# Optimization experiments

Measured on AMD Instinct MI355X. Metric: run time of the kernel, lower is better.

The kernel has to match this reference:

```python
import jax, jax.numpy as jnp
import numpy as np

B = 384          # batch; must equal F for the final broadcast to be valid
F = 384          # out_features
H = 64           # hidden_dim
TAU = 1.0        # d_k passed to attention()
EPS = 1e-12      # F.normalize eps


def _l2_normalize(x):
    # torch F.normalize(p=2, dim=-1): x / max(||x||, eps)
    n = jnp.sqrt(jnp.sum(x * x, axis=-1, keepdims=True))
    return x / jnp.maximum(n, EPS)


def setup_inputs() -> dict:
    key = jax.random.key(0)
    kx, kwq, kbq, kwk, kbk = jax.random.split(key, 5)
    bound = 1.0 / np.sqrt(F)  # torch Linear default init range
    x = jax.random.normal(kx, (B, F), dtype=jnp.float32)
    Wq = jax.random.uniform(kwq, (F * H, F), jnp.float32, -bound, bound)
    bq = jax.random.uniform(kbq, (F * H,), jnp.float32, -bound, bound)
    Wk = jax.random.uniform(kwk, (F * H, F), jnp.float32, -bound, bound)
    bk = jax.random.uniform(kbk, (F * H,), jnp.float32, -bound, bound)
    return {"x": x, "Wq": Wq, "bq": bq, "Wk": Wk, "bk": bk}


def reference(x, Wq, bq, Wk, bk):
    # q = qs(x), k = ks(x): [B, F*H] -> reshape [B, F, H]
    q = (x @ Wq.T + bq).reshape(B, F, H)
    k = (x @ Wk.T + bk).reshape(B, F, H)
    # L2-normalized QK attention with temperature sqrt(tau)
    q = _l2_normalize(q)
    k = _l2_normalize(k)
    scores = jnp.einsum('bfh,bgh->bfg', q, k) / jnp.sqrt(jnp.float32(TAU))
    scores = jax.nn.softmax(scores, axis=-1)  # [B, F, F]
    # faithful to `input * scores`: x[B,F] left-pads to [1,B,F]; valid since B==F
    return x * scores
```

## Files before the change

### kernel.cpp

```cpp
#include <hip/hip_runtime.h>
#include <hip/hip_bf16.h>


typedef __attribute__((ext_vector_type(8))) short bf16x8;
typedef __attribute__((ext_vector_type(4))) float f32x4;

__device__ __forceinline__ ushort f2bf(float f) {
  union { __hip_bfloat16 h; ushort u; } c;
  c.h = __float2bfloat16(f);
  return c.u;
}

__device__ __forceinline__ void load_lds16(const void* g, void* l) {
  __builtin_amdgcn_global_load_lds(
      (const __attribute__((address_space(1))) void*)g,
      (__attribute__((address_space(3))) void*)l, 16, 0, 0);
}

__global__ __launch_bounds__(256) void xconv(const float* __restrict__ xin,
                                             ushort* __restrict__ xbf) {
  int t = blockIdx.x * 256 + threadIdx.x;
  int o = t * 8;
  int kt = o / 12288;
  int rem = o - kt * 12288;
  int m = rem >> 5;
  int sp = (rem >> 3) & 3;
  int slot = sp ^ ((m >> 1) & 3);
  const float* src = xin + m * 384 + kt * 32 + slot * 8;
  float4 a = *reinterpret_cast<const float4*>(src);
  float4 b = *reinterpret_cast<const float4*>(src + 4);
  ushort4 u0 = make_ushort4(f2bf(a.x), f2bf(a.y), f2bf(a.z), f2bf(a.w));
  ushort4 u1 = make_ushort4(f2bf(b.x), f2bf(b.y), f2bf(b.z), f2bf(b.w));
  *reinterpret_cast<ushort4*>(xbf + o)     = u0;
  *reinterpret_cast<ushort4*>(xbf + o + 4) = u1;
}

__global__ __launch_bounds__(256) void qk_gemm(
    const ushort* __restrict__ xbf,
    const float* __restrict__ Wq, const float* __restrict__ bq,
    const float* __restrict__ Wk, const float* __restrict__ bk,
    ushort* __restrict__ qhat, ushort* __restrict__ khat)
{
  const int bx = blockIdx.x;
  const int n0 = bx * 64;
  const float* W    = blockIdx.y ? Wk : Wq;
  const float* bias = blockIdx.y ? bk : bq;
  ushort* outp      = blockIdx.y ? khat : qhat;

  __shared__ __align__(16) ushort Alds[384 * 32];
  __shared__ __align__(16) ushort Blds[64 * 40];

  const int tid  = threadIdx.x;
  const int wave = tid >> 6;
  const int lane = tid & 63;
  const int l15  = lane & 15;
  const int lhi  = lane >> 4;

  f32x4 acc[6][4];
  #pragma unroll
  for (int m = 0; m < 6; ++m)
    #pragma unroll
    for (int n = 0; n < 4; ++n) acc[m][n] = (f32x4)(0.f);

  const int aslot = lhi ^ ((l15 >> 1) & 3);

  for (int kt = 0; kt < 12; ++kt) {
    const ushort* asrc = xbf + kt * 12288 + lane * 8;
    #pragma unroll
    for (int i = 0; i < 6; ++i) {
      int chunk = wave * 6 + i;
      load_lds16(asrc + chunk * 512, (char*)Alds + chunk * 1024);
    }
    #pragma unroll
    for (int i = 0; i < 2; ++i) {
      int idx = tid + 256 * i;
      int row = idx >> 3, c4 = idx & 7;
      float4 v = *reinterpret_cast<const float4*>(
          W + (size_t)(n0 + row) * 384 + kt * 32 + c4 * 4);
      ushort4 u = make_ushort4(f2bf(v.x), f2bf(v.y), f2bf(v.z), f2bf(v.w));
      *reinterpret_cast<ushort4*>(&Blds[row * 40 + c4 * 4]) = u;
    }
    __syncthreads();

    bf16x8 bfr[4];
    #pragma unroll
    for (int nf = 0; nf < 4; ++nf)
      bfr[nf] = *reinterpret_cast<const bf16x8*>(&Blds[(nf * 16 + l15) * 40 + lhi * 8]);
    #pragma unroll
    for (int mf = 0; mf < 6; ++mf) {
      int rr = wave * 96 + mf * 16 + l15;
      bf16x8 afr = *reinterpret_cast<const bf16x8*>(&Alds[rr * 32 + aslot * 8]);
      #pragma unroll
      for (int nf = 0; nf < 4; ++nf)
        acc[mf][nf] = __builtin_amdgcn_mfma_f32_16x16x32_bf16(afr, bfr[nf], acc[mf][nf], 0, 0, 0);
    }
    __syncthreads();
  }

  float bv[4];
  #pragma unroll
  for (int nf = 0; nf < 4; ++nf) bv[nf] = bias[n0 + nf * 16 + l15];

  float scl[6][4];
  #pragma unroll
  for (int mf = 0; mf < 6; ++mf) {
    float ss[4];
    #pragma unroll
    for (int j = 0; j < 4; ++j) {
      float s = 0.f;
      #pragma unroll
      for (int nf = 0; nf < 4; ++nf) {
        float v = acc[mf][nf][j] + bv[nf];
        acc[mf][nf][j] = v;
        s += v * v;
      }
      ss[j] = s;
    }
    #pragma unroll
    for (int m = 1; m < 16; m <<= 1) {
      #pragma unroll
      for (int j = 0; j < 4; ++j) ss[j] += __shfl_xor(ss[j], m, 64);
    }
    #pragma unroll
    for (int j = 0; j < 4; ++j)
      scl[mf][j] = 1.f / fmaxf(sqrtf(ss[j]), 1e-12f);
  }

  const int sw = bx & 7;
  ushort* E = Alds + wave * 3072;
  #pragma unroll
  for (int hh = 0; hh < 2; ++hh) {
    __syncthreads();
    #pragma unroll
    for (int lmf = 0; lmf < 3; ++lmf) {
      const int mf = hh * 3 + lmf;
      #pragma unroll
      for (int nf = 0; nf < 4; ++nf)
        #pragma unroll
        for (int j = 0; j < 4; ++j)
          E[(lmf * 16 + lhi * 4 + j) * 64 + nf * 16 + l15] =
              f2bf(acc[mf][nf][j] * scl[mf][j]);
    }
    __syncthreads();
    #pragma unroll
    for (int i = 0; i < 6; ++i) {
      int lr = i * 8 + (lane >> 3);
      int q  = lane & 7;
      bf16x8 v = *reinterpret_cast<const bf16x8*>(&E[lr * 64 + ((q ^ sw) << 3)]);
      int grow = wave * 96 + hh * 48 + lr;
      *reinterpret_cast<bf16x8*>(outp + (size_t)grow * 24576 + n0 + q * 8) = v;
    }
  }
}

#define PSTR 392
__global__ __launch_bounds__(256, 3) void attn_out(
    const float* __restrict__ xin,
    const ushort* __restrict__ qhat,
    const ushort* __restrict__ khat,
    float* __restrict__ out)
{
  const int id  = blockIdx.x;
  const int xcd = id & 7;
  const int j_  = id >> 3;
  const int b   = xcd * 48 + j_ / 6;
  const int f0  = (j_ % 6) * 64;

  __shared__ __align__(16) char smem[32 * PSTR * 4];
  ushort* Klds = reinterpret_cast<ushort*>(smem);
  float*  Slds = reinterpret_cast<float*>(smem);

  const int tid  = threadIdx.x;
  const int wave = tid >> 6;
  const int lane = tid & 63;
  const int l15  = lane & 15;
  const int lhi  = lane >> 4;

  const int fr = f0 + wave * 16 + l15;
  bf16x8 q8[2];
  #pragma unroll
  for (int ks = 0; ks < 2; ++ks)
    q8[ks] = *reinterpret_cast<const bf16x8*>(
        qhat + (size_t)b * 24576 + (size_t)fr * 64 + (((ks * 4 + lhi) ^ (l15 & 7)) << 3));
  __builtin_amdgcn_sched_barrier(0);

  const ushort* ksrc = khat + (size_t)b * 24576 + lane * 8;
  #pragma unroll
  for (int i = 0; i < 6; ++i) {
    int chunk = wave + 4 * i;
    load_lds16(ksrc + chunk * 512, (char*)Klds + chunk * 1024);
  }
  __builtin_amdgcn_sched_barrier(0);
  #pragma unroll
  for (int i = 6; i < 12; ++i) {
    int chunk = wave + 4 * i;
    load_lds16(ksrc + chunk * 512, (char*)Klds + chunk * 1024);
  }

  f32x4 acc[24];
  #pragma unroll
  for (int n = 0; n < 24; ++n) acc[n] = (f32x4)(0.f);

  asm volatile("s_waitcnt vmcnt(6)" ::: "memory");
  __builtin_amdgcn_s_barrier();
  __builtin_amdgcn_sched_barrier(0);
  #pragma unroll
  for (int ks = 0; ks < 2; ++ks) {
    #pragma unroll
    for (int nf = 0; nf < 12; ++nf) {
      bf16x8 kf = *reinterpret_cast<const bf16x8*>(
          &Klds[(nf * 16 + l15) * 64 + (((ks * 4 + lhi) ^ (l15 & 7)) << 3)]);
      acc[nf] = __builtin_amdgcn_mfma_f32_16x16x32_bf16(kf, q8[ks], acc[nf], 0, 0, 0);
    }
  }
  asm volatile("s_waitcnt vmcnt(0)" ::: "memory");
  __builtin_amdgcn_s_barrier();
  __builtin_amdgcn_sched_barrier(0);
  #pragma unroll
  for (int ks = 0; ks < 2; ++ks) {
    #pragma unroll
    for (int nf = 12; nf < 24; ++nf) {
      bf16x8 kf = *reinterpret_cast<const bf16x8*>(
          &Klds[(nf * 16 + l15) * 64 + (((ks * 4 + lhi) ^ (l15 & 7)) << 3)]);
      acc[nf] = __builtin_amdgcn_mfma_f32_16x16x32_bf16(kf, q8[ks], acc[nf], 0, 0, 0);
    }
  }

  float m0 = acc[0][0], m1 = acc[0][1], m2 = acc[0][2], m3 = acc[0][3];
  #pragma unroll
  for (int nf = 1; nf < 24; ++nf) {
    m0 = fmaxf(m0, acc[nf][0]); m1 = fmaxf(m1, acc[nf][1]);
    m2 = fmaxf(m2, acc[nf][2]); m3 = fmaxf(m3, acc[nf][3]);
  }
  float m = fmaxf(fmaxf(m0, m1), fmaxf(m2, m3));
  m = fmaxf(m, __shfl_xor(m, 16, 64));
  m = fmaxf(m, __shfl_xor(m, 32, 64));

  float s0 = 0.f, s1 = 0.f, s2 = 0.f, s3 = 0.f;
  #pragma unroll
  for (int nf = 0; nf < 24; ++nf) {
    float p0 = __expf(acc[nf][0] - m);
    float p1 = __expf(acc[nf][1] - m);
    float p2 = __expf(acc[nf][2] - m);
    float p3 = __expf(acc[nf][3] - m);
    acc[nf][0] = p0; acc[nf][1] = p1; acc[nf][2] = p2; acc[nf][3] = p3;
    s0 += p0; s1 += p1; s2 += p2; s3 += p3;
  }
  float s = (s0 + s1) + (s2 + s3);
  s += __shfl_xor(s, 16, 64);
  s += __shfl_xor(s, 32, 64);
  const float inv = 1.f / s;

  __syncthreads();

  #pragma unroll
  for (int half = 0; half < 2; ++half) {
    if ((wave >> 1) == half) {
      const int prow = (wave & 1) * 16 + l15;
      #pragma unroll
      for (int nf = 0; nf < 24; ++nf) {
        f32x4 v;
        v[0] = acc[nf][0] * inv; v[1] = acc[nf][1] * inv;
        v[2] = acc[nf][2] * inv; v[3] = acc[nf][3] * inv;
        *reinterpret_cast<f32x4*>(&Slds[prow * PSTR + nf * 16 + lhi * 4]) = v;
      }
    }
    __syncthreads();

    const int rbase = f0 + half * 32;
    const float* xsrc = xin + (size_t)rbase * 384;
    float* odst = out + (size_t)b * 147456 + (size_t)rbase * 384;
    #pragma unroll
    for (int i = 0; i < 12; ++i) {
      int idx = tid + 256 * i;
      int row = idx / 96, c = idx - row * 96;
      float4 p4 = *reinterpret_cast<const float4*>(&Slds[row * PSTR + c * 4]);
      float4 x4 = *reinterpret_cast<const float4*>(xsrc + row * 384 + c * 4);
      float4 o;
      o.x = x4.x * p4.x;  o.y = x4.y * p4.y;
      o.z = x4.z * p4.z;  o.w = x4.w * p4.w;
      *reinterpret_cast<float4*>(odst + row * 384 + c * 4) = o;
    }
    if (half == 0) __syncthreads();
  }
}

extern "C" void kernel_launch(void* const* d_in, const int* in_sizes, int n_in,
                              void* d_out, int out_size, void* d_ws, size_t ws_size,
                              hipStream_t stream) {
  const float* x  = (const float*)d_in[0];
  const float* Wq = (const float*)d_in[1];
  const float* bq = (const float*)d_in[2];
  const float* Wk = (const float*)d_in[3];
  const float* bk = (const float*)d_in[4];
  float* out = (float*)d_out;

  ushort* qhat = (ushort*)d_ws;
  ushort* khat = qhat + (size_t)384 * 24576;
  ushort* xbf  = khat + (size_t)384 * 24576;

  xconv<<<dim3(72), dim3(256), 0, stream>>>(x, xbf);

  dim3 g1(384, 2), b1(256);
  qk_gemm<<<g1, b1, 0, stream>>>(xbf, Wq, bq, Wk, bk, qhat, khat);

  attn_out<<<dim3(2304), dim3(256), 0, stream>>>(x, qhat, khat, out);
}
```

Baseline: 115.4 us.

## Software-pipeline the QK projection GEMM with double-buffered weight tiles and register prefetch

```diff
diff --git a/kernel.cpp b/kernel.cpp
--- a/kernel.cpp
+++ b/kernel.cpp
@@ -48,7 +48,7 @@
   ushort* outp      = blockIdx.y ? khat : qhat;
 
   __shared__ __align__(16) ushort Alds[384 * 32];
-  __shared__ __align__(16) ushort Blds[64 * 40];
+  __shared__ __align__(16) ushort Blds[2][64 * 40];
 
   const int tid  = threadIdx.x;
   const int wave = tid >> 6;
@@ -56,6 +56,10 @@
   const int l15  = lane & 15;
   const int lhi  = lane >> 4;
 
+  const int wrow = tid >> 3;
+  const int wc4  = (tid & 7) * 4;
+  const float* Wbase = W + (size_t)(n0 + wrow) * 384 + wc4;
+
   f32x4 acc[6][4];
   #pragma unroll
   for (int m = 0; m < 6; ++m)
@@ -64,38 +68,86 @@
 
   const int aslot = lhi ^ ((l15 >> 1) & 3);
 
-  for (int kt = 0; kt < 12; ++kt) {
-    const ushort* asrc = xbf + kt * 12288 + lane * 8;
+  float4 sXa, sXb, sYa, sYb;
+  sXa = *reinterpret_cast<const float4*>(Wbase);
+  sXb = *reinterpret_cast<const float4*>(Wbase + 32 * 384);
+  sYa = *reinterpret_cast<const float4*>(Wbase + 32);
+  sYb = *reinterpret_cast<const float4*>(Wbase + 32 * 384 + 32);
+  {
+    ushort4 u0 = make_ushort4(f2bf(sXa.x), f2bf(sXa.y), f2bf(sXa.z), f2bf(sXa.w));
+    ushort4 u1 = make_ushort4(f2bf(sXb.x), f2bf(sXb.y), f2bf(sXb.z), f2bf(sXb.w));
+    *reinterpret_cast<ushort4*>(&Blds[0][wrow * 40 + wc4])        = u0;
+    *reinterpret_cast<ushort4*>(&Blds[0][(wrow + 32) * 40 + wc4]) = u1;
+    const ushort* asrc = xbf + lane * 8;
     #pragma unroll
     for (int i = 0; i < 6; ++i) {
       int chunk = wave * 6 + i;
       load_lds16(asrc + chunk * 512, (char*)Alds + chunk * 1024);
     }
-    #pragma unroll
-    for (int i = 0; i < 2; ++i) {
-      int idx = tid + 256 * i;
-      int row = idx >> 3, c4 = idx & 7;
-      float4 v = *reinterpret_cast<const float4*>(
-          W + (size_t)(n0 + row) * 384 + kt * 32 + c4 * 4);
-      ushort4 u = make_ushort4(f2bf(v.x), f2bf(v.y), f2bf(v.z), f2bf(v.w));
-      *reinterpret_cast<ushort4*>(&Blds[row * 40 + c4 * 4]) = u;
-    }
-    __syncthreads();
-
-    bf16x8 bfr[4];
-    #pragma unroll
-    for (int nf = 0; nf < 4; ++nf)
-      bfr[nf] = *reinterpret_cast<const bf16x8*>(&Blds[(nf * 16 + l15) * 40 + lhi * 8]);
-    #pragma unroll
-    for (int mf = 0; mf < 6; ++mf) {
-      int rr = wave * 96 + mf * 16 + l15;
-      bf16x8 afr = *reinterpret_cast<const bf16x8*>(&Alds[rr * 32 + aslot * 8]);
-      #pragma unroll
-      for (int nf = 0; nf < 4; ++nf)
-        acc[mf][nf] = __builtin_amdgcn_mfma_f32_16x16x32_bf16(afr, bfr[nf], acc[mf][nf], 0, 0, 0);
-    }
-    __syncthreads();
-  }
+    sXa = *reinterpret_cast<const float4*>(Wbase + 2 * 32);
+    sXb = *reinterpret_cast<const float4*>(Wbase + 2 * 32 + 32 * 384);
+  }
+  asm volatile("s_waitcnt lgkmcnt(0)" ::: "memory");
+  __builtin_amdgcn_s_barrier();
+
+#define GEMM_STEP(kt, Sa, Sb)                                                   \
+  {                                                                             \
+                  \
+    asm volatile("s_waitcnt vmcnt(2)" ::: "memory");                            \
+    const ushort* Bc = Blds[(kt) & 1];                                          \
+    bf16x8 bfr[4];                                                              \
+    _Pragma("unroll")                                                           \
+    for (int nf = 0; nf < 4; ++nf)                                              \
+      bfr[nf] = *reinterpret_cast<const bf16x8*>(                               \
+          &Bc[(nf * 16 + l15) * 40 + lhi * 8]);                                 \
+    bf16x8 afr[6];                                                              \
+    _Pragma("unroll")                                                           \
+    for (int mf = 0; mf < 6; ++mf)                                              \
+      afr[mf] = *reinterpret_cast<const bf16x8*>(                               \
+          &Alds[(wave * 96 + mf * 16 + l15) * 32 + aslot * 8]);                 \
+                 \
+    asm volatile("s_waitcnt lgkmcnt(0)" ::: "memory");                          \
+    {                                                                           \
+      int ka = (kt) + 1 <= 11 ? (kt) + 1 : 11;                                  \
+      const ushort* asrc = xbf + ka * 12288 + lane * 8;                         \
+      _Pragma("unroll")                                                         \
+      for (int i = 0; i < 6; ++i) {                                             \
+        int chunk = wave * 6 + i;                                               \
+        load_lds16(asrc + chunk * 512, (char*)Alds + chunk * 1024);             \
+      }                                                                         \
+    }                                                                           \
+         \
+    {                                                                           \
+      ushort* Bn = Blds[((kt) + 1) & 1];                                        \
+      ushort4 u0 = make_ushort4(f2bf(Sa.x), f2bf(Sa.y), f2bf(Sa.z), f2bf(Sa.w));\
+      ushort4 u1 = make_ushort4(f2bf(Sb.x), f2bf(Sb.y), f2bf(Sb.z), f2bf(Sb.w));\
+      *reinterpret_cast<ushort4*>(&Bn[wrow * 40 + wc4])        = u0;            \
+      *reinterpret_cast<ushort4*>(&Bn[(wrow + 32) * 40 + wc4]) = u1;            \
+    }                                                                           \
+                \
+    {                                                                           \
+      int ktp = (kt) + 3 <= 11 ? (kt) + 3 : 11;                                 \
+      Sa = *reinterpret_cast<const float4*>(Wbase + ktp * 32);                  \
+      Sb = *reinterpret_cast<const float4*>(Wbase + ktp * 32 + 32 * 384);       \
+    }                                                                           \
+    _Pragma("unroll")                                                           \
+    for (int mf = 0; mf < 6; ++mf)                                              \
+      _Pragma("unroll")                                                         \
+      for (int nf = 0; nf < 4; ++nf)                                            \
+        acc[mf][nf] = __builtin_amdgcn_mfma_f32_16x16x32_bf16(                  \
+            afr[mf], bfr[nf], acc[mf][nf], 0, 0, 0);                            \
+                          \
+    asm volatile("s_waitcnt lgkmcnt(0)" ::: "memory");                          \
+    __builtin_amdgcn_s_barrier();                                               \
+  }
+
+  for (int kt2 = 0; kt2 < 12; kt2 += 2) {
+    GEMM_STEP(kt2,     sYa, sYb)
+    GEMM_STEP(kt2 + 1, sXa, sXb)
+  }
+#undef GEMM_STEP
+
+  asm volatile("s_waitcnt vmcnt(0)" ::: "memory");
 
   float bv[4];
   #pragma unroll
```

Result: slower. 121.8 us (+5.6%).
